# Kernel optimization log

Measured on AMD Instinct MI355X. Metric: run time of the kernel, lower is better.

Reference implementation:

```python
import jax, jax.numpy as jnp
import numpy as np

BATCH, L, DM, DS, K, EXPAND = 4, 2048, 1024, 16, 4, 2
DI = EXPAND * DM  # 2048


def setup_inputs() -> dict:
    key = jax.random.key(0)
    ks = jax.random.split(key, 12)
    s = 0.02  # small init so exp(exp(dt)*A) and tanh stay well-behaved
    return {
        "x": jax.random.normal(ks[0], (BATCH, L, DM), jnp.float32),
        "W_in": jax.random.normal(ks[1], (2 * DI, DM), jnp.float32) * s,
        "b_in": jax.random.normal(ks[2], (2 * DI,), jnp.float32) * s,
        "conv_w": jax.random.normal(ks[3], (DI, 1, K), jnp.float32) * s,  # depthwise
        "conv_b": jax.random.normal(ks[4], (DI,), jnp.float32) * s,
        "W_x": jax.random.normal(ks[5], (2 * DS, DI), jnp.float32) * s,
        "b_x": jax.random.normal(ks[6], (2 * DS,), jnp.float32) * s,
        "dt": jax.random.normal(ks[7], (DI,), jnp.float32) * s,
        "A": jax.random.normal(ks[8], (DS, DS), jnp.float32) * s,
        "D": jnp.ones((DI,), jnp.float32),
        "W_out": jax.random.normal(ks[9], (DM, DI), jnp.float32) * s,
        "b_out": jax.random.normal(ks[10], (DM,), jnp.float32) * s,
    }


def _forward(x, W_in, b_in, conv_w, conv_b, W_x, b_x, dt, A, D, W_out, b_out):
    # in_proj: (B, L, 2*DI), split into conv path and residual
    xr = x @ W_in.T + b_in
    xi, res = jnp.split(xr, 2, axis=-1)
    # depthwise causal conv1d: torch pads both sides by K-1 then truncates to L,
    # equivalent to left-pad-only causal conv
    xc = jax.lax.conv_general_dilated(
        xi.transpose(0, 2, 1), conv_w, window_strides=(1,),
        padding=((K - 1, 0),), feature_group_count=DI,
        dimension_numbers=("NCH", "OIH", "NCH"))
    xc = (xc + conv_b[None, :, None]).transpose(0, 2, 1)  # (B, L, DI)
    xs = jax.nn.silu(xc)
    # x_proj -> B, C (each (B, L, DS))
    bc = xs @ W_x.T + b_x
    Bm, Cm = jnp.split(bc, 2, axis=-1)
    # dt = exp(self.dt) sliced to first DS entries, indexed per step by i % DS
    dtv = jnp.exp(dt)[:DS]
    dt_seq = dtv[jnp.arange(L) % DS]  # (L,)
    # NOTE: torch code computes x * D inside _selective_scan but never uses it;
    # the scan output depends only on dt, A, B, C.

    def step(h, inp):
        d_i, B_t, C_t = inp  # scalar, (B, DS), (B, DS)
        A_t = jnp.exp(d_i * A)  # (DS, DS)
        h_new = jnp.tanh(jnp.einsum("ij,bj->bi", A_t, h) + B_t * h + C_t)
        return h_new, h_new

    h0 = jnp.zeros((x.shape[0], DS), x.dtype)
    _, hs = jax.lax.scan(step, h0, (dt_seq, Bm.transpose(1, 0, 2), Cm.transpose(1, 0, 2)))
    hs = hs.transpose(1, 0, 2)  # (B, L, DS)
    y = jnp.tile(hs, (1, 1, DI // DS)) + res  # repeat state to d_inner, add res
    return y @ W_out.T + b_out


def reference(x, W_in, b_in, conv_w, conv_b, W_x, b_x, dt, A, D, W_out, b_out):
    return _forward(x, W_in, b_in, conv_w, conv_b, W_x, b_x, dt, A, D, W_out, b_out)
```

## Files before the change

### kernel.cpp

```cpp
#include <hip/hip_runtime.h>
#include <cstdint>
#include <cstddef>

typedef __attribute__((ext_vector_type(4))) float f32x4;
typedef __attribute__((ext_vector_type(8))) __bf16 bf16x8;
typedef __attribute__((ext_vector_type(4))) unsigned int u32x4;
typedef __attribute__((ext_vector_type(2))) unsigned int u32x2;

#define DEVFN static __device__ __forceinline__

#define OFF_XBF    0ull
#define OFF_WINBF  16777216ull
#define OFF_WXBF   20971520ull
#define OFF_WOUTBF 21102592ull
#define OFF_WRT    25296896ull
#define OFF_WC     29491200ull
#define OFF_WRED   31588352ull
#define OFF_BCONST 31653888ull
#define OFF_XIBF   31657984ull
#define OFF_XSBF   65212416ull
#define OFF_BC     98766848ull
#define OFF_HS     99815424ull

DEVFN unsigned short f2bf(float f) {
  unsigned u = __float_as_uint(f);
  return (unsigned short)((u + 0x7FFFu + ((u >> 16) & 1u)) >> 16);
}

DEVFN void gload_lds16(const void* g, void* l) {
  __builtin_amdgcn_global_load_lds(
      (const __attribute__((address_space(1))) void*)g,
      (__attribute__((address_space(3))) void*)l, 16, 0, 0);
}

#define DPPF(x, ctrl) \
  __int_as_float(__builtin_amdgcn_update_dpp(0, __float_as_int(x), ctrl, 0xF, 0xF, true))

DEVFN void cvt8(const float* __restrict__ in, unsigned short* __restrict__ out, int t) {
  f32x4 a = *(const f32x4*)(in + (size_t)t * 8);
  f32x4 b = *(const f32x4*)(in + (size_t)t * 8 + 4);
  u32x4 r;
  r.x = (unsigned)f2bf(a[0]) | ((unsigned)f2bf(a[1]) << 16);
  r.y = (unsigned)f2bf(a[2]) | ((unsigned)f2bf(a[3]) << 16);
  r.z = (unsigned)f2bf(b[0]) | ((unsigned)f2bf(b[1]) << 16);
  r.w = (unsigned)f2bf(b[2]) | ((unsigned)f2bf(b[3]) << 16);
  *(u32x4*)(out + (size_t)t * 8) = r;
}

__global__ __launch_bounds__(256) void k_prep(
    const float* __restrict__ x, const float* __restrict__ W_in,
    const float* __restrict__ W_x, const float* __restrict__ W_out,
    const float* __restrict__ b_in, const float* __restrict__ b_out,
    unsigned short* __restrict__ xbf, unsigned short* __restrict__ winbf,
    unsigned short* __restrict__ wxbf, unsigned short* __restrict__ woutbf,
    unsigned short* __restrict__ wrtbf, float* __restrict__ wred,
    float* __restrict__ bconst) {
  const int bid = blockIdx.x, tid = threadIdx.x;
  if (bid < 4096)      { cvt8(x,     xbf,    bid * 256 + tid); return; }
  if (bid < 5120)      { cvt8(W_in,  winbf,  (bid - 4096) * 256 + tid); return; }
  if (bid < 5152)      { cvt8(W_x,   wxbf,   (bid - 5120) * 256 + tid); return; }
  if (bid < 6176)      { cvt8(W_out, woutbf, (bid - 5152) * 256 + tid); return; }
  if (bid < 6240) {
    const int t = (bid - 6176) * 256 + tid;
    const int m = t >> 4, j = t & 15;
    float s = 0.f;
    for (int r = 0; r < 128; r++) s += W_out[(size_t)m * 2048 + r * 16 + j];
    wred[t] = s;
    return;
  }
  if (bid < 6256) {
    const int t = (bid - 6240) * 256 + tid;
    const int m = t >> 2, q = t & 3;
    const float* wr = W_out + (size_t)m * 2048 + q * 512;
    const float* bi = b_in + 2048 + q * 512;
    float s = 0.f;
    for (int j = 0; j < 128; j++) {
      const f32x4 w = *(const f32x4*)(wr + j * 4);
      const f32x4 v = *(const f32x4*)(bi + j * 4);
      s += w[0]*v[0] + w[1]*v[1] + w[2]*v[2] + w[3]*v[3];
    }
    s += DPPF(s, 0xB1);
    s += DPPF(s, 0x4E);
    if ((tid & 3) == 0) bconst[m] = b_out[m] + s;
    return;
  }
  __shared__ float lt[64][65];
  const int tt = bid - 6256;
  const int d0 = (tt >> 4) * 64, k0 = (tt & 15) * 64;
  const int r16 = tid >> 4, c4 = tid & 15;
#pragma unroll
  for (int i = 0; i < 4; i++) {
    const int dr = r16 + i * 16;
    const f32x4 v = *(const f32x4*)(W_in + (size_t)(2048 + d0 + dr) * 1024 + k0 + c4 * 4);
    lt[dr][c4 * 4 + 0] = v[0]; lt[dr][c4 * 4 + 1] = v[1];
    lt[dr][c4 * 4 + 2] = v[2]; lt[dr][c4 * 4 + 3] = v[3];
  }
  __syncthreads();
#pragma unroll
  for (int i = 0; i < 4; i++) {
    const int kr = r16 + i * 16;
    u32x2 rr;
    rr.x = (unsigned)f2bf(lt[c4 * 4 + 0][kr]) | ((unsigned)f2bf(lt[c4 * 4 + 1][kr]) << 16);
    rr.y = (unsigned)f2bf(lt[c4 * 4 + 2][kr]) | ((unsigned)f2bf(lt[c4 * 4 + 3][kr]) << 16);
    *(u32x2*)(wrtbf + (size_t)(k0 + kr) * 2048 + d0 + c4 * 4) = rr;
  }
}

template <int EPI>
DEVFN void gemm128(const unsigned short* __restrict__ Ag,
                   const unsigned short* __restrict__ Bg, int K,
                   int m0, int n0, const float* __restrict__ bias,
                   float* __restrict__ outf, unsigned short* __restrict__ outbf) {
  __shared__ unsigned short As[128 * 64];
  __shared__ unsigned short Bs[128 * 64];
  const int tid = threadIdx.x;
  const int wave = tid >> 6, lane = tid & 63;
  const int wm = wave >> 1, wn = wave & 1;
  const int fr = lane & 15;
  const int k8 = (lane >> 4) << 3;

  f32x4 acc[4][4];
#pragma unroll
  for (int a = 0; a < 4; a++)
#pragma unroll
    for (int b = 0; b < 4; b++) acc[a][b] = f32x4{0.f, 0.f, 0.f, 0.f};

  for (int kt = 0; kt < K; kt += 64) {
#pragma unroll
    for (int i = 0; i < 4; i++) {
      const int base = (wave << 10) + (i << 12);
      const int off = base + (lane << 4);
      const int row = off >> 7;
      const int col = (off & 127) >> 1;
      gload_lds16(Ag + (size_t)(m0 + row) * K + kt + col, (char*)As + base);
      gload_lds16(Bg + (size_t)(n0 + row) * K + kt + col, (char*)Bs + base);
    }
    __syncthreads();
#pragma unroll
    for (int kk = 0; kk < 2; kk++) {
      bf16x8 af[4], bfr[4];
#pragma unroll
      for (int f = 0; f < 4; f++) {
        af[f]  = *(const bf16x8*)&As[(wm * 64 + f * 16 + fr) * 64 + kk * 32 + k8];
        bfr[f] = *(const bf16x8*)&Bs[(wn * 64 + f * 16 + fr) * 64 + kk * 32 + k8];
      }
#pragma unroll
      for (int fi = 0; fi < 4; fi++)
#pragma unroll
        for (int fj = 0; fj < 4; fj++)
          acc[fi][fj] = __builtin_amdgcn_mfma_f32_16x16x32_bf16(
              af[fi], bfr[fj], acc[fi][fj], 0, 0, 0);
    }
    __syncthreads();
  }

  const int r0 = (lane >> 4) * 4;
#pragma unroll
  for (int fj = 0; fj < 4; fj++) {
    const int col = n0 + wn * 64 + fj * 16 + fr;
    const float bia = (EPI == 2) ? 0.f : bias[col];
#pragma unroll
    for (int fi = 0; fi < 4; fi++) {
      const int rowb = m0 + wm * 64 + fi * 16 + r0;
#pragma unroll
      for (int r = 0; r < 4; r++) {
        const float v = acc[fi][fj][r] + bia;
        if (EPI == 0)      outbf[(size_t)(rowb + r) * 2048 + col] = f2bf(v);
        else if (EPI == 1) outf[(size_t)(rowb + r) * 1024 + col] = v;
        else               outbf[(size_t)(rowb + r) * 1024 + col] = f2bf(v);
      }
    }
  }
}

__global__ __launch_bounds__(256) void k_wc(const unsigned short* __restrict__ woutbf,
                                            const unsigned short* __restrict__ wrtbf,
                                            unsigned short* __restrict__ wcbf) {
  const int bid = blockIdx.x;
  gemm128<2>(woutbf, wrtbf, 2048, (bid >> 3) * 128, (bid & 7) * 128, nullptr,
             nullptr, wcbf);
}

__global__ __launch_bounds__(256) void k_gemm1(const unsigned short* __restrict__ xbf,
                                               const unsigned short* __restrict__ winbf,
                                               const float* __restrict__ b_in,
                                               unsigned short* __restrict__ xibf) {
  const int bid = blockIdx.x;
  gemm128<0>(xbf, winbf, 1024, (bid >> 4) * 128, (bid & 15) * 128, b_in, nullptr, xibf);
}

__global__ __launch_bounds__(256) void k_conv(const unsigned short* __restrict__ xi,
                                              const float* __restrict__ cw,
                                              const float* __restrict__ cb,
                                              unsigned short* __restrict__ xs) {
  const int t = blockIdx.x * 256 + threadIdx.x;
  const int c4 = t & 511;
  const int lc = (t >> 9) & 255;
  const int b  = t >> 17;
  const int l0 = lc * 8;
  const int c0 = c4 * 4;
  const unsigned short* xb = xi + ((size_t)(b * 2048 + l0)) * 2048 + c0;
  u32x2 raw[11];
#pragma unroll
  for (int j = 0; j < 11; j++) {
    const int l = l0 + j - 3;
    raw[j] = (l >= 0) ? *(const u32x2*)(xb + ((long)j - 3) * 2048) : u32x2{0u, 0u};
  }
  f32x4 val[11];
#pragma unroll
  for (int j = 0; j < 11; j++) {
    val[j][0] = __uint_as_float(raw[j].x << 16);
    val[j][1] = __uint_as_float(raw[j].x & 0xFFFF0000u);
    val[j][2] = __uint_as_float(raw[j].y << 16);
    val[j][3] = __uint_as_float(raw[j].y & 0xFFFF0000u);
  }
  const f32x4 w0 = *(const f32x4*)(cw + (size_t)c0 * 4);
  const f32x4 w1 = *(const f32x4*)(cw + (size_t)(c0 + 1) * 4);
  const f32x4 w2 = *(const f32x4*)(cw + (size_t)(c0 + 2) * 4);
  const f32x4 w3 = *(const f32x4*)(cw + (size_t)(c0 + 3) * 4);
  const f32x4 bb = *(const f32x4*)(cb + c0);
  unsigned short* xp = xs + ((size_t)(b * 2048 + l0)) * 2048 + c0;
#pragma unroll
  for (int jo = 0; jo < 8; jo++) {
    f32x4 v;
    v[0] = bb[0] + w0[0]*val[jo][0] + w0[1]*val[jo+1][0] + w0[2]*val[jo+2][0] + w0[3]*val[jo+3][0];
    v[1] = bb[1] + w1[0]*val[jo][1] + w1[1]*val[jo+1][1] + w1[2]*val[jo+2][1] + w1[3]*val[jo+3][1];
    v[2] = bb[2] + w2[0]*val[jo][2] + w2[1]*val[jo+1][2] + w2[2]*val[jo+2][2] + w2[3]*val[jo+3][2];
    v[3] = bb[3] + w3[0]*val[jo][3] + w3[1]*val[jo+1][3] + w3[2]*val[jo+2][3] + w3[3]*val[jo+3][3];
#pragma unroll
    for (int q = 0; q < 4; q++) {
      const float x = v[q];
      v[q] = x * __builtin_amdgcn_rcpf(1.f + __expf(-x));
    }
    u32x2 rr;
    rr.x = (unsigned)f2bf(v[0]) | ((unsigned)f2bf(v[1]) << 16);
    rr.y = (unsigned)f2bf(v[2]) | ((unsigned)f2bf(v[3]) << 16);
    *(u32x2*)(xp + (size_t)jo * 2048) = rr;
  }
}

__global__ __launch_bounds__(256) void k_gemm2(const unsigned short* __restrict__ xs,
                                               const unsigned short* __restrict__ wx,
                                               const float* __restrict__ bx,
                                               float* __restrict__ bc) {
  __shared__ unsigned short As[128 * 64];
  __shared__ unsigned short Bs[32 * 64];
  const int tid = threadIdx.x, wave = tid >> 6, lane = tid & 63;
  const int m0 = blockIdx.x * 128;
  const int fr = lane & 15, k8 = (lane >> 4) << 3;
  f32x4 acc[2][2];
#pragma unroll
  for (int a = 0; a < 2; a++)
#pragma unroll
    for (int b = 0; b < 2; b++) acc[a][b] = f32x4{0.f, 0.f, 0.f, 0.f};

  for (int kt = 0; kt < 2048; kt += 64) {
#pragma unroll
    for (int i = 0; i < 4; i++) {
      const int base = (wave << 10) + (i << 12);
      const int off = base + (lane << 4);
      const int row = off >> 7, col = (off & 127) >> 1;
      gload_lds16(xs + (size_t)(m0 + row) * 2048 + kt + col, (char*)As + base);
    }
    {
      const int base = (wave << 10);
      const int off = base + (lane << 4);
      const int row = off >> 7, col = (off & 127) >> 1;
      gload_lds16(wx + (size_t)row * 2048 + kt + col, (char*)Bs + base);
    }
    __syncthreads();
#pragma unroll
    for (int kk = 0; kk < 2; kk++) {
      bf16x8 af[2], bfr[2];
#pragma unroll
      for (int f = 0; f < 2; f++) {
        af[f]  = *(const bf16x8*)&As[(wave * 32 + f * 16 + fr) * 64 + kk * 32 + k8];
        bfr[f] = *(const bf16x8*)&Bs[(f * 16 + fr) * 64 + kk * 32 + k8];
      }
#pragma unroll
      for (int fi = 0; fi < 2; fi++)
#pragma unroll
        for (int fj = 0; fj < 2; fj++)
          acc[fi][fj] = __builtin_amdgcn_mfma_f32_16x16x32_bf16(
              af[fi], bfr[fj], acc[fi][fj], 0, 0, 0);
    }
    __syncthreads();
  }
  const int r0 = (lane >> 4) * 4;
#pragma unroll
  for (int fi = 0; fi < 2; fi++)
#pragma unroll
    for (int fj = 0; fj < 2; fj++) {
      const int col = fj * 16 + fr;
      const float bia = bx[col];
#pragma unroll
      for (int r = 0; r < 4; r++) {
        const int row = m0 + wave * 32 + fi * 16 + r0 + r;
        bc[(size_t)row * 32 + col] = acc[fi][fj][r] + bia;
      }
    }
}

DEVFN float scan4_step(float h, const f32x4 ax, float Bt, float Ct, int a0) {
  const int hv = __float_as_int(h);
  const float g0 = __int_as_float(__builtin_amdgcn_ds_bpermute(a0,      hv));
  const float g1 = __int_as_float(__builtin_amdgcn_ds_bpermute(a0 + 16, hv));
  const float g2 = __int_as_float(__builtin_amdgcn_ds_bpermute(a0 + 32, hv));
  const float g3 = __int_as_float(__builtin_amdgcn_ds_bpermute(a0 + 48, hv));
  const float pa = fmaf(ax[1], g1, ax[0] * g0);
  const float pb = fmaf(ax[3], g3, ax[2] * g2);
  float p = pa + pb;
  p += DPPF(p, 0xB1);
  p += DPPF(p, 0x4E);
  const float s = p + fmaf(Bt, h, Ct);
  const float e = __expf(2.f * s);
  return fmaf(-2.f, __builtin_amdgcn_rcpf(e + 1.f), 1.f);
}

__global__ __launch_bounds__(256) void k4_gemm_scan(
    const unsigned short* __restrict__ xbf, const unsigned short* __restrict__ wcbf,
    const float* __restrict__ bconst, float* __restrict__ out,
    const float* __restrict__ bc, const float* __restrict__ dt,
    const float* __restrict__ Amat, float* __restrict__ hs) {
  if (blockIdx.x < 512) {
    const int bid = blockIdx.x;
    gemm128<1>(xbf, wcbf, 1024, (bid >> 3) * 128, (bid & 7) * 128, bconst,
               out, nullptr);
    return;
  }
  const int tid = threadIdx.x;
  const int b = tid >> 6;
  const int lane = tid & 63;
  const int i = lane >> 2, k = lane & 3;

  const f32x4 arow = *(const f32x4*)(Amat + i * 16 + k * 4);
  f32x4 axv[16];
#pragma unroll
  for (int p = 0; p < 16; p++) {
    const float e = __expf(dt[p]);
    axv[p][0] = __expf(e * arow[0]);
    axv[p][1] = __expf(e * arow[1]);
    axv[p][2] = __expf(e * arow[2]);
    axv[p][3] = __expf(e * arow[3]);
  }
  const int a0 = (lane & 3) << 6;
  const float* bcp = bc + (size_t)b * 65536 + i;
  float* hsp = hs + (size_t)b * 32768 + i;
  float h = 0.f;

  float p0B[8], p0C[8], p1B[8], p1C[8];
#pragma unroll
  for (int q = 0; q < 8; q++) { p0B[q] = bcp[q * 32]; p0C[q] = bcp[q * 32 + 16]; }

  for (int l0 = 0; l0 < 2048; l0 += 16) {
    {
      const float* bq = bcp + (size_t)(l0 + 8) * 32;
#pragma unroll
      for (int q = 0; q < 8; q++) { p1B[q] = bq[q * 32]; p1C[q] = bq[q * 32 + 16]; }
    }
#pragma unroll
    for (int q = 0; q < 8; q++) {
      h = scan4_step(h, axv[q], p0B[q], p0C[q], a0);
      if (k == 0) hsp[(size_t)(l0 + q) * 16] = h;
    }
    {
      const float* bq = bcp + (size_t)((l0 + 16) & 2047) * 32;
#pragma unroll
      for (int q = 0; q < 8; q++) { p0B[q] = bq[q * 32]; p0C[q] = bq[q * 32 + 16]; }
    }
#pragma unroll
    for (int q = 8; q < 16; q++) {
      h = scan4_step(h, axv[q], p1B[q - 8], p1C[q - 8], a0);
      if (k == 0) hsp[(size_t)(l0 + q) * 16] = h;
    }
  }
}

__global__ __launch_bounds__(256) void k5_combine(float* __restrict__ out,
                                                  const float* __restrict__ hs,
                                                  const float* __restrict__ wred) {
  const int m4 = threadIdx.x;
  const int rg = blockIdx.x;
  f32x4 w[4][4];
#pragma unroll
  for (int mi = 0; mi < 4; mi++)
#pragma unroll
    for (int q = 0; q < 4; q++)
      w[mi][q] = *(const f32x4*)&wred[(size_t)(m4 * 4 + mi) * 16 + q * 4];
#pragma unroll
  for (int r = 0; r < 4; r++) {
    const size_t row = (size_t)rg * 4 + r;
    f32x4 hv[4];
#pragma unroll
    for (int q = 0; q < 4; q++) hv[q] = *(const f32x4*)&hs[row * 16 + q * 4];
    float* op = out + row * 1024 + m4 * 4;
    f32x4 o = *(f32x4*)op;
#pragma unroll
    for (int mi = 0; mi < 4; mi++) {
      float v = 0.f;
#pragma unroll
      for (int q = 0; q < 4; q++)
        v += w[mi][q][0]*hv[q][0] + w[mi][q][1]*hv[q][1] +
             w[mi][q][2]*hv[q][2] + w[mi][q][3]*hv[q][3];
      o[mi] += v;
    }
    *(f32x4*)op = o;
  }
}

extern "C" void kernel_launch(void* const* d_in, const int* in_sizes, int n_in,
                              void* d_out, int out_size, void* d_ws, size_t ws_size,
                              hipStream_t stream) {
  const float* x      = (const float*)d_in[0];
  const float* W_in   = (const float*)d_in[1];
  const float* b_in   = (const float*)d_in[2];
  const float* conv_w = (const float*)d_in[3];
  const float* conv_b = (const float*)d_in[4];
  const float* W_x    = (const float*)d_in[5];
  const float* b_x    = (const float*)d_in[6];
  const float* dt     = (const float*)d_in[7];
  const float* A      = (const float*)d_in[8];
  const float* W_out  = (const float*)d_in[10];
  const float* b_out  = (const float*)d_in[11];
  float* out = (float*)d_out;

  char* ws = (char*)d_ws;
  unsigned short* xbf    = (unsigned short*)(ws + OFF_XBF);
  unsigned short* winbf  = (unsigned short*)(ws + OFF_WINBF);
  unsigned short* wxbf   = (unsigned short*)(ws + OFF_WXBF);
  unsigned short* woutbf = (unsigned short*)(ws + OFF_WOUTBF);
  unsigned short* wrtbf  = (unsigned short*)(ws + OFF_WRT);
  unsigned short* wcbf   = (unsigned short*)(ws + OFF_WC);
  float*          wred   = (float*)(ws + OFF_WRED);
  float*          bconst = (float*)(ws + OFF_BCONST);
  unsigned short* xibf   = (unsigned short*)(ws + OFF_XIBF);
  unsigned short* xsbf   = (unsigned short*)(ws + OFF_XSBF);
  float*          bc     = (float*)(ws + OFF_BC);
  float*          hsb    = (float*)(ws + OFF_HS);

  k_prep<<<6768, 256, 0, stream>>>(x, W_in, W_x, W_out, b_in, b_out,
                                   xbf, winbf, wxbf, woutbf, wrtbf, wred, bconst);
  k_wc<<<64, 256, 0, stream>>>(woutbf, wrtbf, wcbf);
  k_gemm1<<<1024, 256, 0, stream>>>(xbf, winbf, b_in, xibf);
  k_conv<<<2048, 256, 0, stream>>>(xibf, conv_w, conv_b, xsbf);
  k_gemm2<<<64, 256, 0, stream>>>(xsbf, wxbf, b_x, bc);
  k4_gemm_scan<<<513, 256, 0, stream>>>(xbf, wcbf, bconst, out, bc, dt, A, hsb);
  k5_combine<<<2048, 256, 0, stream>>>(out, hsb, wred);
}
```

Baseline: 508.4 us.

## Fuse in-proj GEMM, conv, x-proj and scan into one flag-synchronised kernel

Merges the in-proj GEMM, the depthwise conv+SiLU, the x_proj GEMM, the scan and the output GEMM into one persistent-style launch. Ordering between stages comes from per-tile atomic counters and flags instead of kernel boundaries. The conv is now computed on the fly while loading the x_proj A-tile, so the xs intermediate is never written to or read from global memory. The scan starts on each 128-row chunk as soon as its B/C rows are ready, overlapping it with the remaining GEMM work. The risks are spin-waits that depend on block scheduling order, an extra memset per call, and redundant conv work being recomputed inside the GEMM load.

```diff
diff --git a/kernel.cpp b/kernel.cpp
--- a/kernel.cpp
+++ b/kernel.cpp
@@ -8,6 +8,7 @@
 typedef __attribute__((ext_vector_type(2))) unsigned int u32x2;
 
 #define DEVFN static __device__ __forceinline__
+#define AGENT __HIP_MEMORY_SCOPE_AGENT
 
 #define OFF_XBF    0ull
 #define OFF_WINBF  16777216ull
@@ -18,9 +19,9 @@
 #define OFF_WRED   31588352ull
 #define OFF_BCONST 31653888ull
 #define OFF_XIBF   31657984ull
-#define OFF_XSBF   65212416ull
 #define OFF_BC     98766848ull
 #define OFF_HS     99815424ull
+#define OFF_FLAGS  100339712ull
 
 DEVFN unsigned short f2bf(float f) {
   unsigned u = __float_as_uint(f);
@@ -107,12 +108,11 @@
 }
 
 template <int EPI>
-DEVFN void gemm128(const unsigned short* __restrict__ Ag,
+DEVFN void gemm128(unsigned short* __restrict__ As, unsigned short* __restrict__ Bs,
+                   const unsigned short* __restrict__ Ag,
                    const unsigned short* __restrict__ Bg, int K,
                    int m0, int n0, const float* __restrict__ bias,
                    float* __restrict__ outf, unsigned short* __restrict__ outbf) {
-  __shared__ unsigned short As[128 * 64];
-  __shared__ unsigned short Bs[128 * 64];
   const int tid = threadIdx.x;
   const int wave = tid >> 6, lane = tid & 63;
   const int wm = wave >> 1, wn = wave & 1;
@@ -176,129 +176,10 @@
 __global__ __launch_bounds__(256) void k_wc(const unsigned short* __restrict__ woutbf,
                                             const unsigned short* __restrict__ wrtbf,
                                             unsigned short* __restrict__ wcbf) {
+  __shared__ unsigned short sm[128 * 64 * 2];
   const int bid = blockIdx.x;
-  gemm128<2>(woutbf, wrtbf, 2048, (bid >> 3) * 128, (bid & 7) * 128, nullptr,
-             nullptr, wcbf);
-}
-
-__global__ __launch_bounds__(256) void k_gemm1(const unsigned short* __restrict__ xbf,
-                                               const unsigned short* __restrict__ winbf,
-                                               const float* __restrict__ b_in,
-                                               unsigned short* __restrict__ xibf) {
-  const int bid = blockIdx.x;
-  gemm128<0>(xbf, winbf, 1024, (bid >> 4) * 128, (bid & 15) * 128, b_in, nullptr, xibf);
-}
-
-__global__ __launch_bounds__(256) void k_conv(const unsigned short* __restrict__ xi,
-                                              const float* __restrict__ cw,
-                                              const float* __restrict__ cb,
-                                              unsigned short* __restrict__ xs) {
-  const int t = blockIdx.x * 256 + threadIdx.x;
-  const int c4 = t & 511;
-  const int lc = (t >> 9) & 255;
-  const int b  = t >> 17;
-  const int l0 = lc * 8;
-  const int c0 = c4 * 4;
-  const unsigned short* xb = xi + ((size_t)(b * 2048 + l0)) * 2048 + c0;
-  u32x2 raw[11];
-#pragma unroll
-  for (int j = 0; j < 11; j++) {
-    const int l = l0 + j - 3;
-    raw[j] = (l >= 0) ? *(const u32x2*)(xb + ((long)j - 3) * 2048) : u32x2{0u, 0u};
-  }
-  f32x4 val[11];
-#pragma unroll
-  for (int j = 0; j < 11; j++) {
-    val[j][0] = __uint_as_float(raw[j].x << 16);
-    val[j][1] = __uint_as_float(raw[j].x & 0xFFFF0000u);
-    val[j][2] = __uint_as_float(raw[j].y << 16);
-    val[j][3] = __uint_as_float(raw[j].y & 0xFFFF0000u);
-  }
-  const f32x4 w0 = *(const f32x4*)(cw + (size_t)c0 * 4);
-  const f32x4 w1 = *(const f32x4*)(cw + (size_t)(c0 + 1) * 4);
-  const f32x4 w2 = *(const f32x4*)(cw + (size_t)(c0 + 2) * 4);
-  const f32x4 w3 = *(const f32x4*)(cw + (size_t)(c0 + 3) * 4);
-  const f32x4 bb = *(const f32x4*)(cb + c0);
-  unsigned short* xp = xs + ((size_t)(b * 2048 + l0)) * 2048 + c0;
-#pragma unroll
-  for (int jo = 0; jo < 8; jo++) {
-    f32x4 v;
-    v[0] = bb[0] + w0[0]*val[jo][0] + w0[1]*val[jo+1][0] + w0[2]*val[jo+2][0] + w0[3]*val[jo+3][0];
-    v[1] = bb[1] + w1[0]*val[jo][1] + w1[1]*val[jo+1][1] + w1[2]*val[jo+2][1] + w1[3]*val[jo+3][1];
-    v[2] = bb[2] + w2[0]*val[jo][2] + w2[1]*val[jo+1][2] + w2[2]*val[jo+2][2] + w2[3]*val[jo+3][2];
-    v[3] = bb[3] + w3[0]*val[jo][3] + w3[1]*val[jo+1][3] + w3[2]*val[jo+2][3] + w3[3]*val[jo+3][3];
-#pragma unroll
-    for (int q = 0; q < 4; q++) {
-      const float x = v[q];
-      v[q] = x * __builtin_amdgcn_rcpf(1.f + __expf(-x));
-    }
-    u32x2 rr;
-    rr.x = (unsigned)f2bf(v[0]) | ((unsigned)f2bf(v[1]) << 16);
-    rr.y = (unsigned)f2bf(v[2]) | ((unsigned)f2bf(v[3]) << 16);
-    *(u32x2*)(xp + (size_t)jo * 2048) = rr;
-  }
-}
-
-__global__ __launch_bounds__(256) void k_gemm2(const unsigned short* __restrict__ xs,
-                                               const unsigned short* __restrict__ wx,
-                                               const float* __restrict__ bx,
-                                               float* __restrict__ bc) {
-  __shared__ unsigned short As[128 * 64];
-  __shared__ unsigned short Bs[32 * 64];
-  const int tid = threadIdx.x, wave = tid >> 6, lane = tid & 63;
-  const int m0 = blockIdx.x * 128;
-  const int fr = lane & 15, k8 = (lane >> 4) << 3;
-  f32x4 acc[2][2];
-#pragma unroll
-  for (int a = 0; a < 2; a++)
-#pragma unroll
-    for (int b = 0; b < 2; b++) acc[a][b] = f32x4{0.f, 0.f, 0.f, 0.f};
-
-  for (int kt = 0; kt < 2048; kt += 64) {
-#pragma unroll
-    for (int i = 0; i < 4; i++) {
-      const int base = (wave << 10) + (i << 12);
-      const int off = base + (lane << 4);
-      const int row = off >> 7, col = (off & 127) >> 1;
-      gload_lds16(xs + (size_t)(m0 + row) * 2048 + kt + col, (char*)As + base);
-    }
-    {
-      const int base = (wave << 10);
-      const int off = base + (lane << 4);
-      const int row = off >> 7, col = (off & 127) >> 1;
-      gload_lds16(wx + (size_t)row * 2048 + kt + col, (char*)Bs + base);
-    }
-    __syncthreads();
-#pragma unroll
-    for (int kk = 0; kk < 2; kk++) {
-      bf16x8 af[2], bfr[2];
-#pragma unroll
-      for (int f = 0; f < 2; f++) {
-        af[f]  = *(const bf16x8*)&As[(wave * 32 + f * 16 + fr) * 64 + kk * 32 + k8];
-        bfr[f] = *(const bf16x8*)&Bs[(f * 16 + fr) * 64 + kk * 32 + k8];
-      }
-#pragma unroll
-      for (int fi = 0; fi < 2; fi++)
-#pragma unroll
-        for (int fj = 0; fj < 2; fj++)
-          acc[fi][fj] = __builtin_amdgcn_mfma_f32_16x16x32_bf16(
-              af[fi], bfr[fj], acc[fi][fj], 0, 0, 0);
-    }
-    __syncthreads();
-  }
-  const int r0 = (lane >> 4) * 4;
-#pragma unroll
-  for (int fi = 0; fi < 2; fi++)
-#pragma unroll
-    for (int fj = 0; fj < 2; fj++) {
-      const int col = fj * 16 + fr;
-      const float bia = bx[col];
-#pragma unroll
-      for (int r = 0; r < 4; r++) {
-        const int row = m0 + wave * 32 + fi * 16 + r0 + r;
-        bc[(size_t)row * 32 + col] = acc[fi][fj][r] + bia;
-      }
-    }
+  gemm128<2>(sm, sm + 128 * 64, woutbf, wrtbf, 2048,
+             (bid >> 3) * 128, (bid & 7) * 128, nullptr, nullptr, wcbf);
 }
 
 DEVFN float scan4_step(float h, const f32x4 ax, float Bt, float Ct, int a0) {
@@ -317,62 +198,190 @@
   return fmaf(-2.f, __builtin_amdgcn_rcpf(e + 1.f), 1.f);
 }
 
-__global__ __launch_bounds__(256) void k4_gemm_scan(
-    const unsigned short* __restrict__ xbf, const unsigned short* __restrict__ wcbf,
-    const float* __restrict__ bconst, float* __restrict__ out,
-    const float* __restrict__ bc, const float* __restrict__ dt,
-    const float* __restrict__ Amat, float* __restrict__ hs) {
-  if (blockIdx.x < 512) {
-    const int bid = blockIdx.x;
-    gemm128<1>(xbf, wcbf, 1024, (bid >> 3) * 128, (bid & 7) * 128, bconst,
-               out, nullptr);
+__global__ __launch_bounds__(256) void k_mega(
+    const unsigned short* __restrict__ xbf, const unsigned short* __restrict__ winbf,
+    const float* __restrict__ b_in, unsigned short* __restrict__ xibf,
+    const float* __restrict__ cw, const float* __restrict__ cb,
+    const unsigned short* __restrict__ wx, const float* __restrict__ bx,
+    float* __restrict__ bcb,
+    const unsigned short* __restrict__ wcbf, const float* __restrict__ bconst,
+    float* __restrict__ out,
+    const float* __restrict__ dt, const float* __restrict__ Amat,
+    float* __restrict__ hs,
+    int* __restrict__ cnt1, int* __restrict__ flag2) {
+  __shared__ unsigned short sm[128 * 64 * 2];
+  const int bid = blockIdx.x, tid = threadIdx.x;
+
+  if (bid < 1024) {
+    const int m = bid >> 4, n = bid & 15;
+    gemm128<0>(sm, sm + 128 * 64, xbf, winbf, 1024, m * 128, n * 128,
+               b_in, nullptr, xibf);
+    __syncthreads();
+    if (tid == 0)
+      __hip_atomic_fetch_add(&cnt1[m], 1, __ATOMIC_RELEASE, AGENT);
     return;
   }
-  const int tid = threadIdx.x;
-  const int b = tid >> 6;
-  const int lane = tid & 63;
-  const int i = lane >> 2, k = lane & 3;
-
-  const f32x4 arow = *(const f32x4*)(Amat + i * 16 + k * 4);
-  f32x4 axv[16];
-#pragma unroll
-  for (int p = 0; p < 16; p++) {
-    const float e = __expf(dt[p]);
-    axv[p][0] = __expf(e * arow[0]);
-    axv[p][1] = __expf(e * arow[1]);
-    axv[p][2] = __expf(e * arow[2]);
-    axv[p][3] = __expf(e * arow[3]);
-  }
-  const int a0 = (lane & 3) << 6;
-  const float* bcp = bc + (size_t)b * 65536 + i;
-  float* hsp = hs + (size_t)b * 32768 + i;
-  float h = 0.f;
-
-  float p0B[8], p0C[8], p1B[8], p1C[8];
-#pragma unroll
-  for (int q = 0; q < 8; q++) { p0B[q] = bcp[q * 32]; p0C[q] = bcp[q * 32 + 16]; }
-
-  for (int l0 = 0; l0 < 2048; l0 += 16) {
-    {
-      const float* bq = bcp + (size_t)(l0 + 8) * 32;
-#pragma unroll
-      for (int q = 0; q < 8; q++) { p1B[q] = bq[q * 32]; p1C[q] = bq[q * 32 + 16]; }
-    }
-#pragma unroll
-    for (int q = 0; q < 8; q++) {
-      h = scan4_step(h, axv[q], p0B[q], p0C[q], a0);
-      if (k == 0) hsp[(size_t)(l0 + q) * 16] = h;
-    }
-    {
-      const float* bq = bcp + (size_t)((l0 + 16) & 2047) * 32;
-#pragma unroll
-      for (int q = 0; q < 8; q++) { p0B[q] = bq[q * 32]; p0C[q] = bq[q * 32 + 16]; }
-    }
-#pragma unroll
-    for (int q = 8; q < 16; q++) {
-      h = scan4_step(h, axv[q], p1B[q - 8], p1C[q - 8], a0);
-      if (k == 0) hsp[(size_t)(l0 + q) * 16] = h;
-    }
+
+  if (bid < 1088) {
+    unsigned short* As = sm;
+    unsigned short* Bs = sm + 128 * 64;
+    const int m = bid - 1024;
+    const int lt = m & 15;
+    const int m0 = m * 128;
+    while (__hip_atomic_load(&cnt1[m], __ATOMIC_ACQUIRE, AGENT) < 16)
+      __builtin_amdgcn_s_sleep(2);
+    if (lt != 0)
+      while (__hip_atomic_load(&cnt1[m - 1], __ATOMIC_ACQUIRE, AGENT) < 16)
+        __builtin_amdgcn_s_sleep(2);
+
+    const int wave = tid >> 6, lane = tid & 63;
+    const int fr = lane & 15, k8 = (lane >> 4) << 3;
+    f32x4 acc[2][2];
+#pragma unroll
+    for (int a = 0; a < 2; a++)
+#pragma unroll
+      for (int b = 0; b < 2; b++) acc[a][b] = f32x4{0.f, 0.f, 0.f, 0.f};
+
+    for (int kt = 0; kt < 2048; kt += 64) {
+      {
+        const int base = (wave << 10);
+        const int off = base + (lane << 4);
+        const int row = off >> 7, col = (off & 127) >> 1;
+        gload_lds16(wx + (size_t)row * 2048 + kt + col, (char*)Bs + base);
+      }
+#pragma unroll
+      for (int i = 0; i < 4; i++) {
+        const int off = i * 4096 + tid * 16;
+        const int row = off >> 7;
+        const int c8 = (off & 127) >> 1;
+        const int ch = kt + c8;
+        const size_t gb = (size_t)(m0 + row) * 2048 + ch;
+        const int l = (m0 + row) & 2047;
+        u32x4 raw[4];
+#pragma unroll
+        for (int t = 0; t < 4; t++) {
+          const int lsrc = l - 3 + t;
+          raw[t] = (lsrc >= 0) ? *(const u32x4*)(xibf + gb + ((long)t - 3) * 2048)
+                               : u32x4{0u, 0u, 0u, 0u};
+        }
+        u32x4 res;
+        unsigned tmp[4];
+#pragma unroll
+        for (int c = 0; c < 8; c++) {
+          const f32x4 wv = *(const f32x4*)(cw + (size_t)(ch + c) * 4);
+          float a2 = cb[ch + c];
+#pragma unroll
+          for (int t = 0; t < 4; t++) {
+            const unsigned w32 = raw[t][c >> 1];
+            const float xv = __uint_as_float((c & 1) ? (w32 & 0xFFFF0000u) : (w32 << 16));
+            a2 = fmaf(wv[t], xv, a2);
+          }
+          const float sl = a2 * __builtin_amdgcn_rcpf(1.f + __expf(-a2));
+          const unsigned hb = f2bf(sl);
+          if ((c & 1) == 0) tmp[c >> 1] = hb;
+          else              tmp[c >> 1] |= (hb << 16);
+        }
+        res.x = tmp[0]; res.y = tmp[1]; res.z = tmp[2]; res.w = tmp[3];
+        *(u32x4*)((char*)As + off) = res;
+      }
+      __syncthreads();
+#pragma unroll
+      for (int kk = 0; kk < 2; kk++) {
+        bf16x8 af[2], bfr[2];
+#pragma unroll
+        for (int f = 0; f < 2; f++) {
+          af[f]  = *(const bf16x8*)&As[(wave * 32 + f * 16 + fr) * 64 + kk * 32 + k8];
+          bfr[f] = *(const bf16x8*)&Bs[(f * 16 + fr) * 64 + kk * 32 + k8];
+        }
+#pragma unroll
+        for (int fi = 0; fi < 2; fi++)
+#pragma unroll
+          for (int fj = 0; fj < 2; fj++)
+            acc[fi][fj] = __builtin_amdgcn_mfma_f32_16x16x32_bf16(
+                af[fi], bfr[fj], acc[fi][fj], 0, 0, 0);
+      }
+      __syncthreads();
+    }
+    const int r0 = (lane >> 4) * 4;
+#pragma unroll
+    for (int fi = 0; fi < 2; fi++)
+#pragma unroll
+      for (int fj = 0; fj < 2; fj++) {
+        const int col = fj * 16 + fr;
+        const float bia = bx[col];
+#pragma unroll
+        for (int r = 0; r < 4; r++) {
+          const int row = m0 + wave * 32 + fi * 16 + r0 + r;
+          bcb[(size_t)row * 32 + col] = acc[fi][fj][r] + bia;
+        }
+      }
+    __syncthreads();
+    if (tid == 0)
+      __hip_atomic_store(&flag2[m], 1, __ATOMIC_RELEASE, AGENT);
+    return;
+  }
+
+  if (bid == 1088) {
+    const int b = tid >> 6;
+    const int lane = tid & 63;
+    const int i = lane >> 2, k = lane & 3;
+    const f32x4 arow = *(const f32x4*)(Amat + i * 16 + k * 4);
+    f32x4 axv[16];
+#pragma unroll
+    for (int p = 0; p < 16; p++) {
+      const float e = __expf(dt[p]);
+      axv[p][0] = __expf(e * arow[0]);
+      axv[p][1] = __expf(e * arow[1]);
+      axv[p][2] = __expf(e * arow[2]);
+      axv[p][3] = __expf(e * arow[3]);
+    }
+    const int a0 = (lane & 3) << 6;
+    const float* bcp = bcb + (size_t)b * 65536 + i;
+    float* hsp = hs + (size_t)b * 32768 + i;
+    float h = 0.f;
+    float pB0[8], pC0[8], pB1[8], pC1[8];
+
+    for (int c = 0; c < 16; ++c) {
+      const int fidx = (b << 4) + c;
+      while (__hip_atomic_load(&flag2[fidx], __ATOMIC_ACQUIRE, AGENT) == 0)
+        __builtin_amdgcn_s_sleep(2);
+      const int base = c << 7;
+      {
+        const float* bq = bcp + (size_t)base * 32;
+#pragma unroll
+        for (int q = 0; q < 8; q++) { pB0[q] = bq[q * 32]; pC0[q] = bq[q * 32 + 16]; }
+      }
+      for (int g = 0; g < 8; ++g) {
+        const int l0 = base + (g << 4);
+        {
+          const float* bq = bcp + (size_t)(l0 + 8) * 32;
+#pragma unroll
+          for (int q = 0; q < 8; q++) { pB1[q] = bq[q * 32]; pC1[q] = bq[q * 32 + 16]; }
+        }
+#pragma unroll
+        for (int q = 0; q < 8; q++) {
+          h = scan4_step(h, axv[q], pB0[q], pC0[q], a0);
+          if (k == 0) hsp[(size_t)(l0 + q) * 16] = h;
+        }
+        if (g < 7) {
+          const float* bq = bcp + (size_t)(l0 + 16) * 32;
+#pragma unroll
+          for (int q = 0; q < 8; q++) { pB0[q] = bq[q * 32]; pC0[q] = bq[q * 32 + 16]; }
+        }
+#pragma unroll
+        for (int q = 0; q < 8; q++) {
+          h = scan4_step(h, axv[8 + q], pB1[q], pC1[q], a0);
+          if (k == 0) hsp[(size_t)(l0 + 8 + q) * 16] = h;
+        }
+      }
+    }
+    return;
+  }
+
+  {
+    const int bid2 = bid - 1089;
+    gemm128<1>(sm, sm + 128 * 64, xbf, wcbf, 1024,
+               (bid2 >> 3) * 128, (bid2 & 7) * 128, bconst, out, nullptr);
   }
 }
 
@@ -434,16 +443,16 @@
   float*          wred   = (float*)(ws + OFF_WRED);
   float*          bconst = (float*)(ws + OFF_BCONST);
   unsigned short* xibf   = (unsigned short*)(ws + OFF_XIBF);
-  unsigned short* xsbf   = (unsigned short*)(ws + OFF_XSBF);
   float*          bc     = (float*)(ws + OFF_BC);
   float*          hsb    = (float*)(ws + OFF_HS);
-
+  int*            flags  = (int*)(ws + OFF_FLAGS);
+
+  hipMemsetAsync(flags, 0, 2 * 64 * sizeof(int), stream);
   k_prep<<<6768, 256, 0, stream>>>(x, W_in, W_x, W_out, b_in, b_out,
                                    xbf, winbf, wxbf, woutbf, wrtbf, wred, bconst);
   k_wc<<<64, 256, 0, stream>>>(woutbf, wrtbf, wcbf);
-  k_gemm1<<<1024, 256, 0, stream>>>(xbf, winbf, b_in, xibf);
-  k_conv<<<2048, 256, 0, stream>>>(xibf, conv_w, conv_b, xsbf);
-  k_gemm2<<<64, 256, 0, stream>>>(xsbf, wxbf, b_x, bc);
-  k4_gemm_scan<<<513, 256, 0, stream>>>(xbf, wcbf, bconst, out, bc, dt, A, hsb);
+  k_mega<<<1601, 256, 0, stream>>>(xbf, winbf, b_in, xibf, conv_w, conv_b,
+                                   wxbf, b_x, bc, wcbf, bconst, out, dt, A, hsb,
+                                   flags, flags + 64);
   k5_combine<<<2048, 256, 0, stream>>>(out, hsb, wred);
 }
```

New measurement: 646.2 us. 1.27x slower.

## Fuse x_proj, scan and output GEMM into one flag-synchronized kernel

Applied to the files above, without the earlier changes.

Merges the k_wc and gemm1 launches into one grid. The x_proj GEMM, the sequential scan and the output GEMM with the hs-combine epilogue now run as roles in one persistent kernel. Per-tile release/acquire flags let the scan start on each 128-row chunk as soon as its B/C rows exist, and let output tiles finish once their scan chunk is done. This removes several kernel launches and the separate combine pass that reread and rewrote the whole output. The cost is spin-waiting blocks that depend on co-residency and forward progress, plus an extra memset of the flags.

```diff
diff --git a/kernel.cpp b/kernel.cpp
--- a/kernel.cpp
+++ b/kernel.cpp
@@ -8,6 +8,7 @@
 typedef __attribute__((ext_vector_type(2))) unsigned int u32x2;
 
 #define DEVFN static __device__ __forceinline__
+#define AGENT __HIP_MEMORY_SCOPE_AGENT
 
 #define OFF_XBF    0ull
 #define OFF_WINBF  16777216ull
@@ -21,6 +22,7 @@
 #define OFF_XSBF   65212416ull
 #define OFF_BC     98766848ull
 #define OFF_HS     99815424ull
+#define OFF_FLAGS  100339712ull
 
 DEVFN unsigned short f2bf(float f) {
   unsigned u = __float_as_uint(f);
@@ -107,12 +109,11 @@
 }
 
 template <int EPI>
-DEVFN void gemm128(const unsigned short* __restrict__ Ag,
+DEVFN void gemm128(unsigned short* __restrict__ As, unsigned short* __restrict__ Bs,
+                   const unsigned short* __restrict__ Ag,
                    const unsigned short* __restrict__ Bg, int K,
                    int m0, int n0, const float* __restrict__ bias,
-                   float* __restrict__ outf, unsigned short* __restrict__ outbf) {
-  __shared__ unsigned short As[128 * 64];
-  __shared__ unsigned short Bs[128 * 64];
+                   unsigned short* __restrict__ outbf) {
   const int tid = threadIdx.x;
   const int wave = tid >> 6, lane = tid & 63;
   const int wm = wave >> 1, wn = wave & 1;
@@ -158,35 +159,35 @@
 #pragma unroll
   for (int fj = 0; fj < 4; fj++) {
     const int col = n0 + wn * 64 + fj * 16 + fr;
-    const float bia = (EPI == 2) ? 0.f : bias[col];
+    const float bia = (EPI == 0) ? bias[col] : 0.f;
 #pragma unroll
     for (int fi = 0; fi < 4; fi++) {
       const int rowb = m0 + wm * 64 + fi * 16 + r0;
 #pragma unroll
       for (int r = 0; r < 4; r++) {
         const float v = acc[fi][fj][r] + bia;
-        if (EPI == 0)      outbf[(size_t)(rowb + r) * 2048 + col] = f2bf(v);
-        else if (EPI == 1) outf[(size_t)(rowb + r) * 1024 + col] = v;
-        else               outbf[(size_t)(rowb + r) * 1024 + col] = f2bf(v);
-      }
-    }
-  }
-}
-
-__global__ __launch_bounds__(256) void k_wc(const unsigned short* __restrict__ woutbf,
-                                            const unsigned short* __restrict__ wrtbf,
-                                            unsigned short* __restrict__ wcbf) {
+        if (EPI == 0) outbf[(size_t)(rowb + r) * 2048 + col] = f2bf(v);
+        else          outbf[(size_t)(rowb + r) * 1024 + col] = f2bf(v);
+      }
+    }
+  }
+}
+
+__global__ __launch_bounds__(256) void k1_gemm1_wc(
+    const unsigned short* __restrict__ xbf, const unsigned short* __restrict__ winbf,
+    const float* __restrict__ b_in, unsigned short* __restrict__ xibf,
+    const unsigned short* __restrict__ woutbf, const unsigned short* __restrict__ wrtbf,
+    unsigned short* __restrict__ wcbf) {
+  __shared__ unsigned short sm[128 * 64 * 2];
   const int bid = blockIdx.x;
-  gemm128<2>(woutbf, wrtbf, 2048, (bid >> 3) * 128, (bid & 7) * 128, nullptr,
-             nullptr, wcbf);
-}
-
-__global__ __launch_bounds__(256) void k_gemm1(const unsigned short* __restrict__ xbf,
-                                               const unsigned short* __restrict__ winbf,
-                                               const float* __restrict__ b_in,
-                                               unsigned short* __restrict__ xibf) {
-  const int bid = blockIdx.x;
-  gemm128<0>(xbf, winbf, 1024, (bid >> 4) * 128, (bid & 15) * 128, b_in, nullptr, xibf);
+  if (bid < 1024) {
+    gemm128<0>(sm, sm + 8192, xbf, winbf, 1024, (bid >> 4) * 128, (bid & 15) * 128,
+               b_in, xibf);
+  } else {
+    const int t = bid - 1024;
+    gemm128<2>(sm, sm + 8192, woutbf, wrtbf, 2048, (t >> 3) * 128, (t & 7) * 128,
+               nullptr, wcbf);
+  }
 }
 
 __global__ __launch_bounds__(256) void k_conv(const unsigned short* __restrict__ xi,
@@ -237,68 +238,6 @@
     rr.y = (unsigned)f2bf(v[2]) | ((unsigned)f2bf(v[3]) << 16);
     *(u32x2*)(xp + (size_t)jo * 2048) = rr;
   }
-}
-
-__global__ __launch_bounds__(256) void k_gemm2(const unsigned short* __restrict__ xs,
-                                               const unsigned short* __restrict__ wx,
-                                               const float* __restrict__ bx,
-                                               float* __restrict__ bc) {
-  __shared__ unsigned short As[128 * 64];
-  __shared__ unsigned short Bs[32 * 64];
-  const int tid = threadIdx.x, wave = tid >> 6, lane = tid & 63;
-  const int m0 = blockIdx.x * 128;
-  const int fr = lane & 15, k8 = (lane >> 4) << 3;
-  f32x4 acc[2][2];
-#pragma unroll
-  for (int a = 0; a < 2; a++)
-#pragma unroll
-    for (int b = 0; b < 2; b++) acc[a][b] = f32x4{0.f, 0.f, 0.f, 0.f};
-
-  for (int kt = 0; kt < 2048; kt += 64) {
-#pragma unroll
-    for (int i = 0; i < 4; i++) {
-      const int base = (wave << 10) + (i << 12);
-      const int off = base + (lane << 4);
-      const int row = off >> 7, col = (off & 127) >> 1;
-      gload_lds16(xs + (size_t)(m0 + row) * 2048 + kt + col, (char*)As + base);
-    }
-    {
-      const int base = (wave << 10);
-      const int off = base + (lane << 4);
-      const int row = off >> 7, col = (off & 127) >> 1;
-      gload_lds16(wx + (size_t)row * 2048 + kt + col, (char*)Bs + base);
-    }
-    __syncthreads();
-#pragma unroll
-    for (int kk = 0; kk < 2; kk++) {
-      bf16x8 af[2], bfr[2];
-#pragma unroll
-      for (int f = 0; f < 2; f++) {
-        af[f]  = *(const bf16x8*)&As[(wave * 32 + f * 16 + fr) * 64 + kk * 32 + k8];
-        bfr[f] = *(const bf16x8*)&Bs[(f * 16 + fr) * 64 + kk * 32 + k8];
-      }
-#pragma unroll
-      for (int fi = 0; fi < 2; fi++)
-#pragma unroll
-        for (int fj = 0; fj < 2; fj++)
-          acc[fi][fj] = __builtin_amdgcn_mfma_f32_16x16x32_bf16(
-              af[fi], bfr[fj], acc[fi][fj], 0, 0, 0);
-    }
-    __syncthreads();
-  }
-  const int r0 = (lane >> 4) * 4;
-#pragma unroll
-  for (int fi = 0; fi < 2; fi++)
-#pragma unroll
-    for (int fj = 0; fj < 2; fj++) {
-      const int col = fj * 16 + fr;
-      const float bia = bx[col];
-#pragma unroll
-      for (int r = 0; r < 4; r++) {
-        const int row = m0 + wave * 32 + fi * 16 + r0 + r;
-        bc[(size_t)row * 32 + col] = acc[fi][fj][r] + bia;
-      }
-    }
 }
 
 DEVFN float scan4_step(float h, const f32x4 ax, float Bt, float Ct, int a0) {
@@ -317,94 +256,216 @@
   return fmaf(-2.f, __builtin_amdgcn_rcpf(e + 1.f), 1.f);
 }
 
-__global__ __launch_bounds__(256) void k4_gemm_scan(
+__global__ __launch_bounds__(256) void k4_fused(
+    const unsigned short* __restrict__ xsbf, const unsigned short* __restrict__ wx,
+    const float* __restrict__ bx, float* __restrict__ bcb,
     const unsigned short* __restrict__ xbf, const unsigned short* __restrict__ wcbf,
-    const float* __restrict__ bconst, float* __restrict__ out,
-    const float* __restrict__ bc, const float* __restrict__ dt,
-    const float* __restrict__ Amat, float* __restrict__ hs) {
-  if (blockIdx.x < 512) {
-    const int bid = blockIdx.x;
-    gemm128<1>(xbf, wcbf, 1024, (bid >> 3) * 128, (bid & 7) * 128, bconst,
-               out, nullptr);
+    const float* __restrict__ bconst, const float* __restrict__ wred,
+    float* __restrict__ out,
+    const float* __restrict__ dt, const float* __restrict__ Amat,
+    float* __restrict__ hs,
+    int* __restrict__ flag2, int* __restrict__ prog) {
+  __shared__ unsigned short sm[128 * 64 * 2];
+  const int bid = blockIdx.x, tid = threadIdx.x;
+
+  if (bid < 64) {
+    unsigned short* As = sm;
+    unsigned short* Bs = sm + 8192;
+    const int wave = tid >> 6, lane = tid & 63;
+    const int m0 = bid * 128;
+    const int fr = lane & 15, k8 = (lane >> 4) << 3;
+    f32x4 acc[2][2];
+#pragma unroll
+    for (int a = 0; a < 2; a++)
+#pragma unroll
+      for (int b = 0; b < 2; b++) acc[a][b] = f32x4{0.f, 0.f, 0.f, 0.f};
+
+    for (int kt = 0; kt < 2048; kt += 64) {
+#pragma unroll
+      for (int i = 0; i < 4; i++) {
+        const int base = (wave << 10) + (i << 12);
+        const int off = base + (lane << 4);
+        const int row = off >> 7, col = (off & 127) >> 1;
+        gload_lds16(xsbf + (size_t)(m0 + row) * 2048 + kt + col, (char*)As + base);
+      }
+      {
+        const int base = (wave << 10);
+        const int off = base + (lane << 4);
+        const int row = off >> 7, col = (off & 127) >> 1;
+        gload_lds16(wx + (size_t)row * 2048 + kt + col, (char*)Bs + base);
+      }
+      __syncthreads();
+#pragma unroll
+      for (int kk = 0; kk < 2; kk++) {
+        bf16x8 af[2], bfr[2];
+#pragma unroll
+        for (int f = 0; f < 2; f++) {
+          af[f]  = *(const bf16x8*)&As[(wave * 32 + f * 16 + fr) * 64 + kk * 32 + k8];
+          bfr[f] = *(const bf16x8*)&Bs[(f * 16 + fr) * 64 + kk * 32 + k8];
+        }
+#pragma unroll
+        for (int fi = 0; fi < 2; fi++)
+#pragma unroll
+          for (int fj = 0; fj < 2; fj++)
+            acc[fi][fj] = __builtin_amdgcn_mfma_f32_16x16x32_bf16(
+                af[fi], bfr[fj], acc[fi][fj], 0, 0, 0);
+      }
+      __syncthreads();
+    }
+    const int r0 = (lane >> 4) * 4;
+#pragma unroll
+    for (int fi = 0; fi < 2; fi++)
+#pragma unroll
+      for (int fj = 0; fj < 2; fj++) {
+        const int col = fj * 16 + fr;
+        const float bia = bx[col];
+#pragma unroll
+        for (int r = 0; r < 4; r++) {
+          const int row = m0 + wave * 32 + fi * 16 + r0 + r;
+          bcb[(size_t)row * 32 + col] = acc[fi][fj][r] + bia;
+        }
+      }
+    __syncthreads();
+    if (tid == 0)
+      __hip_atomic_store(&flag2[bid], 1, __ATOMIC_RELEASE, AGENT);
     return;
   }
-  const int tid = threadIdx.x;
-  const int b = tid >> 6;
-  const int lane = tid & 63;
-  const int i = lane >> 2, k = lane & 3;
-
-  const f32x4 arow = *(const f32x4*)(Amat + i * 16 + k * 4);
-  f32x4 axv[16];
-#pragma unroll
-  for (int p = 0; p < 16; p++) {
-    const float e = __expf(dt[p]);
-    axv[p][0] = __expf(e * arow[0]);
-    axv[p][1] = __expf(e * arow[1]);
-    axv[p][2] = __expf(e * arow[2]);
-    axv[p][3] = __expf(e * arow[3]);
-  }
-  const int a0 = (lane & 3) << 6;
-  const float* bcp = bc + (size_t)b * 65536 + i;
-  float* hsp = hs + (size_t)b * 32768 + i;
-  float h = 0.f;
-
-  float p0B[8], p0C[8], p1B[8], p1C[8];
-#pragma unroll
-  for (int q = 0; q < 8; q++) { p0B[q] = bcp[q * 32]; p0C[q] = bcp[q * 32 + 16]; }
-
-  for (int l0 = 0; l0 < 2048; l0 += 16) {
-    {
-      const float* bq = bcp + (size_t)(l0 + 8) * 32;
-#pragma unroll
-      for (int q = 0; q < 8; q++) { p1B[q] = bq[q * 32]; p1C[q] = bq[q * 32 + 16]; }
-    }
-#pragma unroll
-    for (int q = 0; q < 8; q++) {
-      h = scan4_step(h, axv[q], p0B[q], p0C[q], a0);
-      if (k == 0) hsp[(size_t)(l0 + q) * 16] = h;
-    }
-    {
-      const float* bq = bcp + (size_t)((l0 + 16) & 2047) * 32;
-#pragma unroll
-      for (int q = 0; q < 8; q++) { p0B[q] = bq[q * 32]; p0C[q] = bq[q * 32 + 16]; }
-    }
-#pragma unroll
-    for (int q = 8; q < 16; q++) {
-      h = scan4_step(h, axv[q], p1B[q - 8], p1C[q - 8], a0);
-      if (k == 0) hsp[(size_t)(l0 + q) * 16] = h;
-    }
-  }
-}
-
-__global__ __launch_bounds__(256) void k5_combine(float* __restrict__ out,
-                                                  const float* __restrict__ hs,
-                                                  const float* __restrict__ wred) {
-  const int m4 = threadIdx.x;
-  const int rg = blockIdx.x;
-  f32x4 w[4][4];
-#pragma unroll
-  for (int mi = 0; mi < 4; mi++)
-#pragma unroll
-    for (int q = 0; q < 4; q++)
-      w[mi][q] = *(const f32x4*)&wred[(size_t)(m4 * 4 + mi) * 16 + q * 4];
-#pragma unroll
-  for (int r = 0; r < 4; r++) {
-    const size_t row = (size_t)rg * 4 + r;
-    f32x4 hv[4];
-#pragma unroll
-    for (int q = 0; q < 4; q++) hv[q] = *(const f32x4*)&hs[row * 16 + q * 4];
-    float* op = out + row * 1024 + m4 * 4;
-    f32x4 o = *(f32x4*)op;
-#pragma unroll
-    for (int mi = 0; mi < 4; mi++) {
-      float v = 0.f;
-#pragma unroll
-      for (int q = 0; q < 4; q++)
-        v += w[mi][q][0]*hv[q][0] + w[mi][q][1]*hv[q][1] +
-             w[mi][q][2]*hv[q][2] + w[mi][q][3]*hv[q][3];
-      o[mi] += v;
-    }
-    *(f32x4*)op = o;
+
+  if (bid == 64) {
+    const int b = tid >> 6;
+    const int lane = tid & 63;
+    const int i = lane >> 2, k = lane & 3;
+    const f32x4 arow = *(const f32x4*)(Amat + i * 16 + k * 4);
+    f32x4 axv[16];
+#pragma unroll
+    for (int p = 0; p < 16; p++) {
+      const float e = __expf(dt[p]);
+      axv[p][0] = __expf(e * arow[0]);
+      axv[p][1] = __expf(e * arow[1]);
+      axv[p][2] = __expf(e * arow[2]);
+      axv[p][3] = __expf(e * arow[3]);
+    }
+    const int a0 = (lane & 3) << 6;
+    const float* bcp = bcb + (size_t)b * 65536 + i;
+    float* hsp = hs + (size_t)b * 32768 + i;
+    float h = 0.f;
+    float pB0[8], pC0[8], pB1[8], pC1[8];
+
+    for (int c = 0; c < 16; ++c) {
+      const int fidx = (b << 4) + c;
+      while (__hip_atomic_load(&flag2[fidx], __ATOMIC_ACQUIRE, AGENT) == 0)
+        __builtin_amdgcn_s_sleep(2);
+      const int base = c << 7;
+      {
+        const float* bq = bcp + (size_t)base * 32;
+#pragma unroll
+        for (int q = 0; q < 8; q++) { pB0[q] = bq[q * 32]; pC0[q] = bq[q * 32 + 16]; }
+      }
+      for (int g = 0; g < 8; ++g) {
+        const int l0 = base + (g << 4);
+        {
+          const float* bq = bcp + (size_t)(l0 + 8) * 32;
+#pragma unroll
+          for (int q = 0; q < 8; q++) { pB1[q] = bq[q * 32]; pC1[q] = bq[q * 32 + 16]; }
+        }
+#pragma unroll
+        for (int q = 0; q < 8; q++) {
+          h = scan4_step(h, axv[q], pB0[q], pC0[q], a0);
+          if (k == 0) hsp[(size_t)(l0 + q) * 16] = h;
+        }
+        if (g < 7) {
+          const float* bq = bcp + (size_t)(l0 + 16) * 32;
+#pragma unroll
+          for (int q = 0; q < 8; q++) { pB0[q] = bq[q * 32]; pC0[q] = bq[q * 32 + 16]; }
+        }
+#pragma unroll
+        for (int q = 0; q < 8; q++) {
+          h = scan4_step(h, axv[8 + q], pB1[q], pC1[q], a0);
+          if (k == 0) hsp[(size_t)(l0 + 8 + q) * 16] = h;
+        }
+      }
+      if (lane == 0)
+        __hip_atomic_store(&prog[fidx], 1, __ATOMIC_RELEASE, AGENT);
+    }
+    return;
+  }
+
+  {
+    const int bid2 = bid - 65;
+    const int mt = bid2 >> 3;
+    const int m0 = mt * 128, n0 = (bid2 & 7) * 128;
+    unsigned short* As = sm;
+    unsigned short* Bs = sm + 8192;
+    const int wave = tid >> 6, lane = tid & 63;
+    const int wm = wave >> 1, wn = wave & 1;
+    const int fr = lane & 15, k8 = (lane >> 4) << 3;
+
+    f32x4 acc[4][4];
+#pragma unroll
+    for (int a = 0; a < 4; a++)
+#pragma unroll
+      for (int b = 0; b < 4; b++) acc[a][b] = f32x4{0.f, 0.f, 0.f, 0.f};
+
+    for (int kt = 0; kt < 1024; kt += 64) {
+#pragma unroll
+      for (int i = 0; i < 4; i++) {
+        const int base = (wave << 10) + (i << 12);
+        const int off = base + (lane << 4);
+        const int row = off >> 7;
+        const int col = (off & 127) >> 1;
+        gload_lds16(xbf + (size_t)(m0 + row) * 1024 + kt + col, (char*)As + base);
+        gload_lds16(wcbf + (size_t)(n0 + row) * 1024 + kt + col, (char*)Bs + base);
+      }
+      __syncthreads();
+#pragma unroll
+      for (int kk = 0; kk < 2; kk++) {
+        bf16x8 af[4], bfr[4];
+#pragma unroll
+        for (int f = 0; f < 4; f++) {
+          af[f]  = *(const bf16x8*)&As[(wm * 64 + f * 16 + fr) * 64 + kk * 32 + k8];
+          bfr[f] = *(const bf16x8*)&Bs[(wn * 64 + f * 16 + fr) * 64 + kk * 32 + k8];
+        }
+#pragma unroll
+        for (int fi = 0; fi < 4; fi++)
+#pragma unroll
+          for (int fj = 0; fj < 4; fj++)
+            acc[fi][fj] = __builtin_amdgcn_mfma_f32_16x16x32_bf16(
+                af[fi], bfr[fj], acc[fi][fj], 0, 0, 0);
+      }
+      __syncthreads();
+    }
+
+    while (__hip_atomic_load(&prog[mt], __ATOMIC_ACQUIRE, AGENT) == 0)
+      __builtin_amdgcn_s_sleep(2);
+
+    const int r0 = (lane >> 4) * 4;
+#pragma unroll
+    for (int fj = 0; fj < 4; fj++) {
+      const int col = n0 + wn * 64 + fj * 16 + fr;
+      const float bia = bconst[col];
+      const f32x4 w0 = *(const f32x4*)&wred[(size_t)col * 16];
+      const f32x4 w1 = *(const f32x4*)&wred[(size_t)col * 16 + 4];
+      const f32x4 w2 = *(const f32x4*)&wred[(size_t)col * 16 + 8];
+      const f32x4 w3 = *(const f32x4*)&wred[(size_t)col * 16 + 12];
+#pragma unroll
+      for (int fi = 0; fi < 4; fi++) {
+        const int rowb = m0 + wm * 64 + fi * 16 + r0;
+#pragma unroll
+        for (int r = 0; r < 4; r++) {
+          const int row = rowb + r;
+          const f32x4 h0 = *(const f32x4*)&hs[(size_t)row * 16];
+          const f32x4 h1 = *(const f32x4*)&hs[(size_t)row * 16 + 4];
+          const f32x4 h2 = *(const f32x4*)&hs[(size_t)row * 16 + 8];
+          const f32x4 h3 = *(const f32x4*)&hs[(size_t)row * 16 + 12];
+          float v = acc[fi][fj][r] + bia;
+          v += w0[0]*h0[0] + w0[1]*h0[1] + w0[2]*h0[2] + w0[3]*h0[3];
+          v += w1[0]*h1[0] + w1[1]*h1[1] + w1[2]*h1[2] + w1[3]*h1[3];
+          v += w2[0]*h2[0] + w2[1]*h2[1] + w2[2]*h2[2] + w2[3]*h2[3];
+          v += w3[0]*h3[0] + w3[1]*h3[1] + w3[2]*h3[2] + w3[3]*h3[3];
+          out[(size_t)row * 1024 + col] = v;
+        }
+      }
+    }
   }
 }
 
@@ -437,13 +498,13 @@
   unsigned short* xsbf   = (unsigned short*)(ws + OFF_XSBF);
   float*          bc     = (float*)(ws + OFF_BC);
   float*          hsb    = (float*)(ws + OFF_HS);
-
+  int*            flags  = (int*)(ws + OFF_FLAGS);
+
+  hipMemsetAsync(flags, 0, 2 * 64 * sizeof(int), stream);
   k_prep<<<6768, 256, 0, stream>>>(x, W_in, W_x, W_out, b_in, b_out,
                                    xbf, winbf, wxbf, woutbf, wrtbf, wred, bconst);
-  k_wc<<<64, 256, 0, stream>>>(woutbf, wrtbf, wcbf);
-  k_gemm1<<<1024, 256, 0, stream>>>(xbf, winbf, b_in, xibf);
+  k1_gemm1_wc<<<1088, 256, 0, stream>>>(xbf, winbf, b_in, xibf, woutbf, wrtbf, wcbf);
   k_conv<<<2048, 256, 0, stream>>>(xibf, conv_w, conv_b, xsbf);
-  k_gemm2<<<64, 256, 0, stream>>>(xsbf, wxbf, b_x, bc);
-  k4_gemm_scan<<<513, 256, 0, stream>>>(xbf, wcbf, bconst, out, bc, dt, A, hsb);
-  k5_combine<<<2048, 256, 0, stream>>>(out, hsb, wred);
-}
+  k4_fused<<<577, 256, 0, stream>>>(xsbf, wxbf, b_x, bc, xbf, wcbf, bconst, wred,
+                                    out, dt, A, hsb, flags, flags + 64);
+}
```

New measurement: 727.1 us. 43.0% more time.
